# Kernel optimization log

Hardware: AMD Instinct MI355X
Metric: run time of the kernel (lower is better)

Reference implementation:

```python
import jax, jax.numpy as jnp
from jax import lax
import numpy as np

B, N, C, H, W = 32, 64, 16, 63, 63  # batch, num_bboxes, num_classes, output H/W


def _conv(x, w, b, s):
    y = lax.conv_general_dilated(x, w, (s, s), 'VALID',
                                 dimension_numbers=('NCHW', 'OIHW', 'NCHW'))
    return y + b[None, :, None, None]


def _bn(x, g, b, eps=1e-5):
    # BatchNorm2d in training mode: batch statistics, biased variance
    m = x.mean((0, 2, 3), keepdims=True)
    v = jnp.mean((x - m) ** 2, (0, 2, 3), keepdims=True)
    return g[None, :, None, None] * (x - m) * lax.rsqrt(v + eps) + b[None, :, None, None]


def _rectangle_render(x):
    # pixel grid flattened with w as the OUTER loop (ww repeated per h), matching torch code
    col = jnp.repeat(jnp.arange(W, dtype=jnp.int32), H)[None, :, None]  # [1,HW,1] x-coord
    row = jnp.tile(jnp.arange(H, dtype=jnp.int32), W)[None, :, None]    # [1,HW,1] y-coord
    c = x[:, :, :4].astype(jnp.int32)  # .long() truncation -> no grad through coords
    xL = c[:, None, :, 0]; yT = c[:, None, :, 1]
    xR = c[:, None, :, 2]; yB = c[:, None, :, 3]
    sub_xL = col - xL; sub_yT = row - yT
    sub_xR = col - xR; sub_yB = row - yB
    sub_y = yB - row;  sub_x = xR - col
    t1 = jnp.clip(sub_yT, 0, 1); t2 = jnp.clip(sub_y, 0, 1)  # relu then cap at 1
    F0 = jnp.maximum(1 - jnp.abs(sub_xL), 0) * t1 * t2
    F1 = jnp.maximum(1 - jnp.abs(sub_xR), 0) * t1 * t2
    t3 = jnp.clip(sub_xL, 0, 1); t4 = jnp.clip(sub_x, 0, 1)
    F2 = jnp.maximum(1 - jnp.abs(sub_yT), 0) * t3 * t4
    F3 = jnp.maximum(1 - jnp.abs(sub_yB), 0) * t3 * t4
    val = jnp.maximum(jnp.maximum(F0, F1), jnp.maximum(F2, F3)).astype(x.dtype)  # [B,HW,N]
    prod = x[:, None, :, 4:] * val[..., None]  # [B,HW,N,C]
    res = prod.max(axis=3)                      # [B,HW,N]
    # view(B,H,W,N).permute(0,1,3,2).permute(0,2,1,3) == reshape + transpose to [B,N,H,W]
    return res.reshape(x.shape[0], H, W, -1).transpose(0, 3, 1, 2)


def setup_inputs() -> dict:
    key = jax.random.key(0)
    ks = jax.random.split(key, 8)
    coords = jax.random.uniform(ks[0], (B, N, 4), jnp.float32) * (W - 1)
    probs = jax.random.uniform(ks[1], (B, N, C), jnp.float32)
    x = jnp.concatenate([coords, probs], axis=2)  # [B, N, 4+C]
    s = 0.05
    return {
        'x': x,
        'conv1_w': jax.random.normal(ks[2], (N, N, 3, 3), jnp.float32) * s,
        'conv1_b': jnp.zeros((N,), jnp.float32),
        'bn1_g': jnp.ones((N,), jnp.float32),
        'bn1_b': jnp.zeros((N,), jnp.float32),
        'conv2_w': jax.random.normal(ks[3], (2 * N, N, 3, 3), jnp.float32) * s,
        'conv2_b': jnp.zeros((2 * N,), jnp.float32),
        'bn2_g': jnp.ones((2 * N,), jnp.float32),
        'bn2_b': jnp.zeros((2 * N,), jnp.float32),
        'conv3_w': jax.random.normal(ks[4], (2 * N, 2 * N, 3, 3), jnp.float32) * s,
        'conv3_b': jnp.zeros((2 * N,), jnp.float32),
        'bn3_g': jnp.ones((2 * N,), jnp.float32),
        'bn3_b': jnp.zeros((2 * N,), jnp.float32),
        'fc1_w': jax.random.normal(ks[5], (N, 2 * N * 49), jnp.float32) * 0.02,
        'fc1_b': jnp.zeros((N,), jnp.float32),
        'fc2_w': jax.random.normal(ks[6], (1, N), jnp.float32) * 0.02,
        'fc2_b': jnp.zeros((1,), jnp.float32),
    }


def reference(x, conv1_w, conv1_b, bn1_g, bn1_b, conv2_w, conv2_b, bn2_g, bn2_b,
              conv3_w, conv3_b, bn3_g, bn3_b, fc1_w, fc1_b, fc2_w, fc2_b):
    layout = _rectangle_render(x)  # [B, N, H, W]
    out = jax.nn.relu(_bn(_conv(layout, conv1_w, conv1_b, 2), bn1_g, bn1_b))
    out = jax.nn.relu(_bn(_conv(out, conv2_w, conv2_b, 2), bn2_g, bn2_b))
    out = jax.nn.relu(_bn(_conv(out, conv3_w, conv3_b, 2), bn3_g, bn3_b))
    out = out.reshape(out.shape[0], -1)  # [B, 2N*49]
    out = jax.nn.relu(out @ fc1_w.T + fc1_b)
    out = out @ fc2_w.T + fc2_b
    return jax.nn.sigmoid(out)  # [B, 1]
```

## Files before the change

### kernel.cpp

```cpp
#include <hip/hip_runtime.h>
#include <math.h>

#define BB 32
#define NREC 64
#define CC 16
#define HW 63

typedef __attribute__((ext_vector_type(8))) short bf16x8;
typedef __attribute__((ext_vector_type(4))) short bf16x4;
typedef __attribute__((ext_vector_type(4))) float f32x4;

__device__ __forceinline__ unsigned short f2b(float x) {
    unsigned u = __float_as_uint(x);
    u += 0x7fffu + ((u >> 16) & 1u);
    return (unsigned short)(u >> 16);
}

__global__ __launch_bounds__(64) void render_nhwc_kernel(const float* __restrict__ x,
                                                         unsigned short* __restrict__ lay) {
    int b = blockIdx.x >> 6;
    int u = blockIdx.x & 63;
    int n = threadIdx.x;
    const float* xp = x + ((size_t)b * 64 + n) * 20;
    int xL = (int)xp[0], yT = (int)xp[1], xR = (int)xp[2], yB = (int)xp[3];
    float m = xp[4];
    #pragma unroll
    for (int c = 1; c < CC; ++c) m = fmaxf(m, xp[4 + c]);
    unsigned short mu = f2b(m);
    unsigned short* op = lay + (((size_t)b * 64 + u) * 64) * 64 + n;
    for (int v = 0; v < 64; ++v) {
        bool vb = (u < HW) && (v < HW) &&
                  (((u == xL || u == xR) && (v > yT && v < yB)) ||
                   ((v == yT || v == yB) && (u > xL && u < xR)));
        op[(size_t)v * 64] = vb ? mu : (unsigned short)0;
    }
}

__global__ __launch_bounds__(256) void wpack_kernel(const float* __restrict__ w,
                                                    unsigned short* __restrict__ wp,
                                                    int COUT, int CIN) {
    int K = CIN * 9;
    int idx = blockIdx.x * 256 + threadIdx.x;
    if (idx >= COUT * K) return;
    int co = idx / K, k = idx - co * K;
    int r = k / CIN, ci = k - r * CIN;
    wp[idx] = f2b(w[((size_t)co * CIN + ci) * 9 + r]);
}

template<int CIN, int COUT, int SR, int SC, int HOUT, int OCP, int RG, int RGP, int MGN>
__global__ __launch_bounds__(256) void gemmconv_kernel(
        const unsigned short* __restrict__ src,
        const unsigned short* __restrict__ wp,
        const float* __restrict__ bias,
        float* __restrict__ out) {
    constexpr int K   = 9 * CIN;
    constexpr int NTB = RGP * OCP / 16;
    constexpr int STR = 2 * RGP + 1;
    constexpr int STC = 2 * OCP + 1;
    constexpr int CIP = 36;
    constexpr int MTB = COUT / 16 / MGN;
    constexpr int NRG = (HOUT + RG - 1) / RG;

    __shared__ unsigned short stage[STR * STC * CIP];

    int tid = threadIdx.x;
    int wv = tid >> 6, lane = tid & 63;
    int l15 = lane & 15, lg = lane >> 4;
    int bid = blockIdx.x;
    int b  = bid & 31;
    int t2 = bid >> 5;
    int rg = t2 % NRG;
    int mg = t2 / NRG;
    int co0 = mg * (COUT / MGN);
    int mw = wv % MTB;

    f32x4 acc[NTB];
    #pragma unroll
    for (int i = 0; i < NTB; ++i) acc[i] = (f32x4){0.f, 0.f, 0.f, 0.f};

    const unsigned short* srcb = src + (size_t)b * SR * SC * CIN;
    int srow0 = 2 * rg * RG;

    for (int cb = 0; cb < CIN / 32; ++cb) {
        __syncthreads();
        for (int idx = tid; idx < STR * STC * 16; idx += 256) {
            int ci2 = idx & 15;
            int rc  = idx >> 4;
            int row = rc / STC, col = rc - row * STC;
            int srow = srow0 + row;
            unsigned v = 0;
            if (srow < SR && col < SC)
                v = *(const unsigned*)(srcb + ((size_t)srow * SC + col) * CIN + cb * 32 + ci2 * 2);
            *(unsigned*)(stage + (row * STC + col) * CIP + ci2 * 2) = v;
        }
        __syncthreads();
        #pragma unroll
        for (int r = 0; r < 9; ++r) {
            int ky = r / 3, kx = r % 3;
            int kk = r * CIN + cb * 32 + lg * 8;
            bf16x8 af = *(const bf16x8*)(wp + (size_t)(co0 + mw * 16 + l15) * K + kk);
            #pragma unroll
            for (int nt = 0; nt < NTB; ++nt) {
                int n = nt * 16 + l15;
                int dy = n / OCP, oxx = n % OCP;
                const unsigned short* sp =
                    stage + ((2 * dy + ky) * STC + (2 * oxx + kx)) * CIP + lg * 8;
                bf16x4 blo = *(const bf16x4*)sp;
                bf16x4 bhi = *(const bf16x4*)(sp + 4);
                bf16x8 bfr;
                bfr[0] = blo[0]; bfr[1] = blo[1]; bfr[2] = blo[2]; bfr[3] = blo[3];
                bfr[4] = bhi[0]; bfr[5] = bhi[1]; bfr[6] = bhi[2]; bfr[7] = bhi[3];
                acc[nt] = __builtin_amdgcn_mfma_f32_16x16x32_bf16(af, bfr, acc[nt], 0, 0, 0);
            }
        }
    }

    #pragma unroll
    for (int nt = 0; nt < NTB; ++nt) {
        int n = nt * 16 + l15;
        int oy = rg * RG + n / OCP, oxx = n % OCP;
        if (oy < HOUT && oxx < HOUT) {
            #pragma unroll
            for (int q = 0; q < 4; ++q) {
                int co = co0 + mw * 16 + lg * 4 + q;
                out[((size_t)b * COUT + co) * (HOUT * HOUT) + oy * HOUT + oxx] =
                    acc[nt][q] + bias[co];
            }
        }
    }
}

__global__ __launch_bounds__(256) void stats_part_kernel(
        const float* __restrict__ raw, float* __restrict__ psum,
        float* __restrict__ psq, int C, int HW2) {
    int c = blockIdx.x / BB;
    int b = blockIdx.x % BB;
    const float* rp = raw + ((size_t)b * C + c) * HW2;
    float s = 0.f, q = 0.f;
    for (int i = threadIdx.x; i < HW2; i += 256) {
        float v = rp[i];
        s += v; q += v * v;
    }
    __shared__ float rs[4], rq[4];
    int lane = threadIdx.x & 63, wv = threadIdx.x >> 6;
    #pragma unroll
    for (int o = 32; o > 0; o >>= 1) { s += __shfl_down(s, o, 64); q += __shfl_down(q, o, 64); }
    if (lane == 0) { rs[wv] = s; rq[wv] = q; }
    __syncthreads();
    if (threadIdx.x == 0) {
        psum[blockIdx.x] = rs[0] + rs[1] + rs[2] + rs[3];
        psq [blockIdx.x] = rq[0] + rq[1] + rq[2] + rq[3];
    }
}

__global__ void stats_fold_kernel(const float* __restrict__ psum,
                                  const float* __restrict__ psq,
                                  const float* __restrict__ g,
                                  const float* __restrict__ be,
                                  float* __restrict__ scale,
                                  float* __restrict__ shift,
                                  int C, float count) {
    int c = threadIdx.x + blockIdx.x * blockDim.x;
    if (c >= C) return;
    float S = 0.f, Q = 0.f;
    for (int b = 0; b < BB; ++b) { S += psum[c * BB + b]; Q += psq[c * BB + b]; }
    float mean = S / count;
    float var  = Q / count - mean * mean;
    float sc   = g[c] * rsqrtf(var + 1e-5f);
    scale[c] = sc;
    shift[c] = be[c] - mean * sc;
}

template<int C, int R, int SCo>
__global__ __launch_bounds__(256) void applyT_kernel(
        const float* __restrict__ raw, const float* __restrict__ scale,
        const float* __restrict__ shift, unsigned short* __restrict__ act) {
    int b = blockIdx.x / R, row = blockIdx.x % R;
    __shared__ float lds[C * (R + 2)];
    for (int idx = threadIdx.x; idx < C * R; idx += 256) {
        int ci = idx / R, col = idx - ci * R;
        float v = fmaxf(fmaf(raw[((size_t)b * C + ci) * (R * R) + row * R + col],
                             scale[ci], shift[ci]), 0.f);
        lds[ci * (R + 2) + col] = v;
    }
    __syncthreads();
    for (int idx = threadIdx.x; idx < SCo * C; idx += 256) {
        int col = idx / C, ci = idx - col * C;
        unsigned short v = 0;
        if (col < R) v = f2b(lds[ci * (R + 2) + col]);
        act[(((size_t)b * R + row) * SCo + col) * C + ci] = v;
    }
}

__global__ __launch_bounds__(64) void apply_kernel(
        const float* __restrict__ raw, const float* __restrict__ scale,
        const float* __restrict__ shift, float* __restrict__ act,
        int C, int HW2) {
    int bc = blockIdx.x;
    int c = bc % C;
    const float* rp = raw + (size_t)bc * HW2;
    float* ap = act + (size_t)bc * HW2;
    float s = scale[c], h = shift[c];
    for (int i = threadIdx.x; i < HW2; i += 64)
        ap[i] = fmaxf(fmaf(rp[i], s, h), 0.f);
}

__global__ __launch_bounds__(256) void fc1_kernel(
        const float* __restrict__ act3, const float* __restrict__ fc1w,
        const float* __restrict__ fc1b, float* __restrict__ h) {
    const int FLAT4 = 6272 / 4;
    int j = blockIdx.x >> 5;
    int b = blockIdx.x & 31;
    const float4* ip = (const float4*)(act3 + (size_t)b * 6272);
    const float4* wp = (const float4*)(fc1w + (size_t)j * 6272);
    float s = 0.f;
    for (int i = threadIdx.x; i < FLAT4; i += 256) {
        float4 xv = ip[i], wv = wp[i];
        s = fmaf(xv.x, wv.x, s); s = fmaf(xv.y, wv.y, s);
        s = fmaf(xv.z, wv.z, s); s = fmaf(xv.w, wv.w, s);
    }
    #pragma unroll
    for (int o = 32; o > 0; o >>= 1) s += __shfl_down(s, o, 64);
    __shared__ float red[4];
    if ((threadIdx.x & 63) == 0) red[threadIdx.x >> 6] = s;
    __syncthreads();
    if (threadIdx.x == 0) {
        float t = red[0] + red[1] + red[2] + red[3];
        h[b * 64 + j] = fmaxf(t + fc1b[j], 0.f);
    }
}

__global__ __launch_bounds__(64) void fc2_kernel(
        const float* __restrict__ h, const float* __restrict__ fc2w,
        const float* __restrict__ fc2b, float* __restrict__ outp) {
    int b = blockIdx.x;
    float v = h[b * 64 + threadIdx.x] * fc2w[threadIdx.x];
    #pragma unroll
    for (int o = 32; o > 0; o >>= 1) v += __shfl_down(v, o, 64);
    if (threadIdx.x == 0) outp[b] = 1.f / (1.f + expf(-(v + fc2b[0])));
}

extern "C" void kernel_launch(void* const* d_in, const int* in_sizes, int n_in,
                              void* d_out, int out_size, void* d_ws, size_t ws_size,
                              hipStream_t stream) {
    const float* x       = (const float*)d_in[0];
    const float* conv1_w = (const float*)d_in[1];
    const float* conv1_b = (const float*)d_in[2];
    const float* bn1_g   = (const float*)d_in[3];
    const float* bn1_b   = (const float*)d_in[4];
    const float* conv2_w = (const float*)d_in[5];
    const float* conv2_b = (const float*)d_in[6];
    const float* bn2_g   = (const float*)d_in[7];
    const float* bn2_b   = (const float*)d_in[8];
    const float* conv3_w = (const float*)d_in[9];
    const float* conv3_b = (const float*)d_in[10];
    const float* bn3_g   = (const float*)d_in[11];
    const float* bn3_b   = (const float*)d_in[12];
    const float* fc1_w   = (const float*)d_in[13];
    const float* fc1_b   = (const float*)d_in[14];
    const float* fc2_w   = (const float*)d_in[15];
    const float* fc2_b   = (const float*)d_in[16];
    float* out = (float*)d_out;

    char* wsc = (char*)d_ws;
    size_t o = 0;
    auto alloc = [&](size_t bytes) { char* p = wsc + o; o += (bytes + 255) & ~(size_t)255; return p; };
    unsigned short* laybf  = (unsigned short*)alloc((size_t)BB * 64 * 64 * 64 * 2);
    unsigned short* act1bf = (unsigned short*)alloc((size_t)BB * 31 * 32 * 64 * 2);
    unsigned short* act2bf = (unsigned short*)alloc((size_t)BB * 15 * 16 * 128 * 2);
    unsigned short* wp1    = (unsigned short*)alloc((size_t)64 * 576 * 2);
    unsigned short* wp2    = (unsigned short*)alloc((size_t)128 * 576 * 2);
    unsigned short* wp3    = (unsigned short*)alloc((size_t)128 * 1152 * 2);
    float* out1   = (float*)alloc((size_t)BB * 64 * 961 * 4);
    float* out2   = (float*)alloc((size_t)BB * 128 * 225 * 4);
    float* out3   = (float*)alloc((size_t)BB * 128 * 49 * 4);
    float* act3   = (float*)alloc((size_t)BB * 128 * 49 * 4);
    float* psum   = (float*)alloc((size_t)128 * BB * 4);
    float* psq    = (float*)alloc((size_t)128 * BB * 4);
    float* scale1 = (float*)alloc(64 * 4);
    float* shift1 = (float*)alloc(64 * 4);
    float* scale2 = (float*)alloc(128 * 4);
    float* shift2 = (float*)alloc(128 * 4);
    float* scale3 = (float*)alloc(128 * 4);
    float* shift3 = (float*)alloc(128 * 4);
    float* hbuf   = (float*)alloc((size_t)BB * 64 * 4);

    wpack_kernel<<<(64 * 576 + 255) / 256, 256, 0, stream>>>(conv1_w, wp1, 64, 64);
    wpack_kernel<<<(128 * 576 + 255) / 256, 256, 0, stream>>>(conv2_w, wp2, 128, 64);
    wpack_kernel<<<(128 * 1152 + 255) / 256, 256, 0, stream>>>(conv3_w, wp3, 128, 128);
    render_nhwc_kernel<<<BB * 64, 64, 0, stream>>>(x, laybf);

    gemmconv_kernel<64, 64, 64, 64, 31, 32, 2, 2, 1>
        <<<32 * 16, 256, 0, stream>>>(laybf, wp1, conv1_b, out1);
    stats_part_kernel<<<64 * BB, 256, 0, stream>>>(out1, psum, psq, 64, 961);
    stats_fold_kernel<<<1, 64, 0, stream>>>(psum, psq, bn1_g, bn1_b, scale1, shift1,
                                            64, (float)(BB * 961));
    applyT_kernel<64, 31, 32><<<BB * 31, 256, 0, stream>>>(out1, scale1, shift1, act1bf);

    gemmconv_kernel<64, 128, 31, 32, 15, 16, 2, 2, 2>
        <<<32 * 16, 256, 0, stream>>>(act1bf, wp2, conv2_b, out2);
    stats_part_kernel<<<128 * BB, 256, 0, stream>>>(out2, psum, psq, 128, 225);
    stats_fold_kernel<<<1, 128, 0, stream>>>(psum, psq, bn2_g, bn2_b, scale2, shift2,
                                             128, (float)(BB * 225));
    applyT_kernel<128, 15, 16><<<BB * 15, 256, 0, stream>>>(out2, scale2, shift2, act2bf);

    gemmconv_kernel<128, 128, 15, 16, 7, 8, 7, 8, 2>
        <<<32 * 2, 256, 0, stream>>>(act2bf, wp3, conv3_b, out3);
    stats_part_kernel<<<128 * BB, 256, 0, stream>>>(out3, psum, psq, 128, 49);
    stats_fold_kernel<<<1, 128, 0, stream>>>(psum, psq, bn3_g, bn3_b, scale3, shift3,
                                             128, (float)(BB * 49));
    apply_kernel<<<BB * 128, 64, 0, stream>>>(out3, scale3, shift3, act3, 128, 49);

    fc1_kernel<<<64 * 32, 256, 0, stream>>>(act3, fc1_w, fc1_b, hbuf);
    fc2_kernel<<<BB, 64, 0, stream>>>(hbuf, fc2_w, fc2_b, out);
}
```

Baseline: 117.1 us.

## Fuse BN stats into conv epilogue and BN apply into next conv's staging

Merges the render and weight-pack kernels into one prep launch. Each conv epilogue now computes per-channel partial sums and squares directly from the accumulators, which removes the separate stats pass. The BN scale/shift, ReLU and bf16 conversion are applied while staging the raw fp32 NCHW input of the next conv, and BN3 is folded into fc1, so the apply/transpose kernels and intermediate activation buffers go away. The cost is that staging now does strided fp32 NCHW loads with per-element scale/shift, and fc1 uses scalar loads with a division per element.

```diff
diff --git a/kernel.cpp b/kernel.cpp
--- a/kernel.cpp
+++ b/kernel.cpp
@@ -2,9 +2,6 @@
 #include <math.h>
 
 #define BB 32
-#define NREC 64
-#define CC 16
-#define HW 63
 
 typedef __attribute__((ext_vector_type(8))) short bf16x8;
 typedef __attribute__((ext_vector_type(4))) short bf16x4;
@@ -16,50 +13,71 @@
     return (unsigned short)(u >> 16);
 }
 
-__global__ __launch_bounds__(64) void render_nhwc_kernel(const float* __restrict__ x,
-                                                         unsigned short* __restrict__ lay) {
-    int b = blockIdx.x >> 6;
-    int u = blockIdx.x & 63;
-    int n = threadIdx.x;
-    const float* xp = x + ((size_t)b * 64 + n) * 20;
-    int xL = (int)xp[0], yT = (int)xp[1], xR = (int)xp[2], yB = (int)xp[3];
-    float m = xp[4];
-    #pragma unroll
-    for (int c = 1; c < CC; ++c) m = fmaxf(m, xp[4 + c]);
-    unsigned short mu = f2b(m);
-    unsigned short* op = lay + (((size_t)b * 64 + u) * 64) * 64 + n;
-    for (int v = 0; v < 64; ++v) {
-        bool vb = (u < HW) && (v < HW) &&
-                  (((u == xL || u == xR) && (v > yT && v < yB)) ||
-                   ((v == yT || v == yB) && (u > xL && u < xR)));
-        op[(size_t)v * 64] = vb ? mu : (unsigned short)0;
-    }
-}
-
-__global__ __launch_bounds__(256) void wpack_kernel(const float* __restrict__ w,
-                                                    unsigned short* __restrict__ wp,
-                                                    int COUT, int CIN) {
-    int K = CIN * 9;
-    int idx = blockIdx.x * 256 + threadIdx.x;
-    if (idx >= COUT * K) return;
-    int co = idx / K, k = idx - co * K;
-    int r = k / CIN, ci = k - r * CIN;
-    wp[idx] = f2b(w[((size_t)co * CIN + ci) * 9 + r]);
-}
-
-template<int CIN, int COUT, int SR, int SC, int HOUT, int OCP, int RG, int RGP, int MGN>
+__global__ __launch_bounds__(256) void prep_kernel(
+        const float* __restrict__ x, unsigned short* __restrict__ lay,
+        const float* __restrict__ w1, const float* __restrict__ w2,
+        const float* __restrict__ w3,
+        unsigned short* __restrict__ wp1, unsigned short* __restrict__ wp2,
+        unsigned short* __restrict__ wp3) {
+    int bid = blockIdx.x;
+    if (bid < 512) {
+        int b = bid >> 4;
+        int u = ((bid & 15) << 2) + (threadIdx.x >> 6);
+        int n = threadIdx.x & 63;
+        const float* xp = x + ((size_t)b * 64 + n) * 20;
+        int xL = (int)xp[0], yT = (int)xp[1], xR = (int)xp[2], yB = (int)xp[3];
+        float m = xp[4];
+        #pragma unroll
+        for (int c = 1; c < 16; ++c) m = fmaxf(m, xp[4 + c]);
+        unsigned short mu = f2b(m);
+        unsigned short* op = lay + (((size_t)b * 64 + u) * 64) * 64 + n;
+        #pragma unroll 4
+        for (int v = 0; v < 64; ++v) {
+            bool vb = (u < 63) && (v < 63) &&
+                      (((u == xL || u == xR) && (v > yT && v < yB)) ||
+                       ((v == yT || v == yB) && (u > xL && u < xR)));
+            op[(size_t)v * 64] = vb ? mu : (unsigned short)0;
+        }
+    } else {
+        int idx = (bid - 512) * 256 + threadIdx.x;
+        const int N1 = 64 * 576, N2 = 128 * 576, N3 = 128 * 1152;
+        if (idx < N1) {
+            int co = idx / 576, k = idx - co * 576;
+            int r = k / 64, ci = k - r * 64;
+            wp1[idx] = f2b(w1[((size_t)co * 64 + ci) * 9 + r]);
+        } else if (idx < N1 + N2) {
+            int i2 = idx - N1;
+            int co = i2 / 576, k = i2 - co * 576;
+            int r = k / 64, ci = k - r * 64;
+            wp2[i2] = f2b(w2[((size_t)co * 64 + ci) * 9 + r]);
+        } else if (idx < N1 + N2 + N3) {
+            int i3 = idx - N1 - N2;
+            int co = i3 / 1152, k = i3 - co * 1152;
+            int r = k / 128, ci = k - r * 128;
+            wp3[i3] = f2b(w3[((size_t)co * 128 + ci) * 9 + r]);
+        }
+    }
+}
+
+template<int CIN, int COUT, int SR, int SC, int HOUT, int OCP, int RG,
+         int RGP, int MGN, bool RAW>
 __global__ __launch_bounds__(256) void gemmconv_kernel(
-        const unsigned short* __restrict__ src,
+        const void* __restrict__ src_,
+        const float* __restrict__ scl,
+        const float* __restrict__ shf,
         const unsigned short* __restrict__ wp,
         const float* __restrict__ bias,
-        float* __restrict__ out) {
-    constexpr int K   = 9 * CIN;
-    constexpr int NTB = RGP * OCP / 16;
-    constexpr int STR = 2 * RGP + 1;
-    constexpr int STC = 2 * OCP + 1;
-    constexpr int CIP = 36;
-    constexpr int MTB = COUT / 16 / MGN;
-    constexpr int NRG = (HOUT + RG - 1) / RG;
+        float* __restrict__ out,
+        float* __restrict__ psum,
+        float* __restrict__ psq) {
+    constexpr int K    = 9 * CIN;
+    constexpr int NTB  = RGP * OCP / 16;
+    constexpr int STR  = 2 * RGP + 1;
+    constexpr int STC  = 2 * OCP + 1;
+    constexpr int CIP  = 36;
+    constexpr int MTB  = COUT / 16 / MGN;
+    constexpr int NRG  = (HOUT + RG - 1) / RG;
+    constexpr int PBLK = BB * NRG;
 
     __shared__ unsigned short stage[STR * STC * CIP];
 
@@ -78,20 +96,38 @@
     #pragma unroll
     for (int i = 0; i < NTB; ++i) acc[i] = (f32x4){0.f, 0.f, 0.f, 0.f};
 
-    const unsigned short* srcb = src + (size_t)b * SR * SC * CIN;
     int srow0 = 2 * rg * RG;
 
     for (int cb = 0; cb < CIN / 32; ++cb) {
         __syncthreads();
-        for (int idx = tid; idx < STR * STC * 16; idx += 256) {
-            int ci2 = idx & 15;
-            int rc  = idx >> 4;
-            int row = rc / STC, col = rc - row * STC;
-            int srow = srow0 + row;
-            unsigned v = 0;
-            if (srow < SR && col < SC)
-                v = *(const unsigned*)(srcb + ((size_t)srow * SC + col) * CIN + cb * 32 + ci2 * 2);
-            *(unsigned*)(stage + (row * STC + col) * CIP + ci2 * 2) = v;
+        if constexpr (RAW) {
+            const float* srcb = (const float*)src_ + (size_t)b * CIN * (SR * SC);
+            for (int idx = tid; idx < 32 * STR * STC; idx += 256) {
+                int ci = idx / (STR * STC);
+                int rc = idx - ci * (STR * STC);
+                int row = rc / STC, col = rc - row * STC;
+                int srow = srow0 + row;
+                int cig = cb * 32 + ci;
+                float v = 0.f;
+                if (srow < SR && col < SC)
+                    v = srcb[((size_t)cig * SR + srow) * SC + col];
+                v = fmaxf(fmaf(v, scl[cig], shf[cig]), 0.f);
+                stage[(row * STC + col) * CIP + ci] = f2b(v);
+            }
+        } else {
+            const unsigned short* srcb =
+                (const unsigned short*)src_ + (size_t)b * SR * SC * CIN;
+            for (int idx = tid; idx < STR * STC * 16; idx += 256) {
+                int ci2 = idx & 15;
+                int rc  = idx >> 4;
+                int row = rc / STC, col = rc - row * STC;
+                int srow = srow0 + row;
+                unsigned v = 0;
+                if (srow < SR && col < SC)
+                    v = *(const unsigned*)(srcb + ((size_t)srow * SC + col) * CIN
+                                           + cb * 32 + ci2 * 2);
+                *(unsigned*)(stage + (row * STC + col) * CIP + ci2 * 2) = v;
+            }
         }
         __syncthreads();
         #pragma unroll
@@ -115,41 +151,37 @@
         }
     }
 
+    float sa[4] = {0.f, 0.f, 0.f, 0.f}, qa[4] = {0.f, 0.f, 0.f, 0.f};
     #pragma unroll
     for (int nt = 0; nt < NTB; ++nt) {
         int n = nt * 16 + l15;
         int oy = rg * RG + n / OCP, oxx = n % OCP;
-        if (oy < HOUT && oxx < HOUT) {
-            #pragma unroll
-            for (int q = 0; q < 4; ++q) {
-                int co = co0 + mw * 16 + lg * 4 + q;
-                out[((size_t)b * COUT + co) * (HOUT * HOUT) + oy * HOUT + oxx] =
-                    acc[nt][q] + bias[co];
-            }
-        }
-    }
-}
-
-__global__ __launch_bounds__(256) void stats_part_kernel(
-        const float* __restrict__ raw, float* __restrict__ psum,
-        float* __restrict__ psq, int C, int HW2) {
-    int c = blockIdx.x / BB;
-    int b = blockIdx.x % BB;
-    const float* rp = raw + ((size_t)b * C + c) * HW2;
-    float s = 0.f, q = 0.f;
-    for (int i = threadIdx.x; i < HW2; i += 256) {
-        float v = rp[i];
-        s += v; q += v * v;
-    }
-    __shared__ float rs[4], rq[4];
-    int lane = threadIdx.x & 63, wv = threadIdx.x >> 6;
-    #pragma unroll
-    for (int o = 32; o > 0; o >>= 1) { s += __shfl_down(s, o, 64); q += __shfl_down(q, o, 64); }
-    if (lane == 0) { rs[wv] = s; rq[wv] = q; }
-    __syncthreads();
-    if (threadIdx.x == 0) {
-        psum[blockIdx.x] = rs[0] + rs[1] + rs[2] + rs[3];
-        psq [blockIdx.x] = rq[0] + rq[1] + rq[2] + rq[3];
+        bool act = (oy < HOUT) && (oxx < HOUT);
+        #pragma unroll
+        for (int q = 0; q < 4; ++q) {
+            int co = co0 + mw * 16 + lg * 4 + q;
+            float v = act ? (acc[nt][q] + bias[co]) : 0.f;
+            if (act)
+                out[((size_t)b * COUT + co) * (HOUT * HOUT) + oy * HOUT + oxx] = v;
+            sa[q] += v; qa[q] += v * v;
+        }
+    }
+    #pragma unroll
+    for (int o = 1; o < 16; o <<= 1) {
+        #pragma unroll
+        for (int q = 0; q < 4; ++q) {
+            sa[q] += __shfl_xor(sa[q], o, 64);
+            qa[q] += __shfl_xor(qa[q], o, 64);
+        }
+    }
+    if (l15 == 0) {
+        int pblk = b * NRG + rg;
+        #pragma unroll
+        for (int q = 0; q < 4; ++q) {
+            int co = co0 + mw * 16 + lg * 4 + q;
+            psum[(size_t)co * PBLK + pblk] = sa[q];
+            psq [(size_t)co * PBLK + pblk] = qa[q];
+        }
     }
 }
 
@@ -159,11 +191,14 @@
                                   const float* __restrict__ be,
                                   float* __restrict__ scale,
                                   float* __restrict__ shift,
-                                  int C, float count) {
+                                  int C, int PBLK, float count) {
     int c = threadIdx.x + blockIdx.x * blockDim.x;
     if (c >= C) return;
     float S = 0.f, Q = 0.f;
-    for (int b = 0; b < BB; ++b) { S += psum[c * BB + b]; Q += psq[c * BB + b]; }
+    for (int p = 0; p < PBLK; ++p) {
+        S += psum[(size_t)c * PBLK + p];
+        Q += psq[(size_t)c * PBLK + p];
+    }
     float mean = S / count;
     float var  = Q / count - mean * mean;
     float sc   = g[c] * rsqrtf(var + 1e-5f);
@@ -171,53 +206,21 @@
     shift[c] = be[c] - mean * sc;
 }
 
-template<int C, int R, int SCo>
-__global__ __launch_bounds__(256) void applyT_kernel(
-        const float* __restrict__ raw, const float* __restrict__ scale,
-        const float* __restrict__ shift, unsigned short* __restrict__ act) {
-    int b = blockIdx.x / R, row = blockIdx.x % R;
-    __shared__ float lds[C * (R + 2)];
-    for (int idx = threadIdx.x; idx < C * R; idx += 256) {
-        int ci = idx / R, col = idx - ci * R;
-        float v = fmaxf(fmaf(raw[((size_t)b * C + ci) * (R * R) + row * R + col],
-                             scale[ci], shift[ci]), 0.f);
-        lds[ci * (R + 2) + col] = v;
-    }
-    __syncthreads();
-    for (int idx = threadIdx.x; idx < SCo * C; idx += 256) {
-        int col = idx / C, ci = idx - col * C;
-        unsigned short v = 0;
-        if (col < R) v = f2b(lds[ci * (R + 2) + col]);
-        act[(((size_t)b * R + row) * SCo + col) * C + ci] = v;
-    }
-}
-
-__global__ __launch_bounds__(64) void apply_kernel(
-        const float* __restrict__ raw, const float* __restrict__ scale,
-        const float* __restrict__ shift, float* __restrict__ act,
-        int C, int HW2) {
-    int bc = blockIdx.x;
-    int c = bc % C;
-    const float* rp = raw + (size_t)bc * HW2;
-    float* ap = act + (size_t)bc * HW2;
-    float s = scale[c], h = shift[c];
-    for (int i = threadIdx.x; i < HW2; i += 64)
-        ap[i] = fmaxf(fmaf(rp[i], s, h), 0.f);
-}
-
 __global__ __launch_bounds__(256) void fc1_kernel(
-        const float* __restrict__ act3, const float* __restrict__ fc1w,
-        const float* __restrict__ fc1b, float* __restrict__ h) {
-    const int FLAT4 = 6272 / 4;
+        const float* __restrict__ out3,
+        const float* __restrict__ scale3, const float* __restrict__ shift3,
+        const float* __restrict__ fc1w,
+        const float* __restrict__ fc1b,
+        float* __restrict__ h) {
     int j = blockIdx.x >> 5;
     int b = blockIdx.x & 31;
-    const float4* ip = (const float4*)(act3 + (size_t)b * 6272);
-    const float4* wp = (const float4*)(fc1w + (size_t)j * 6272);
+    const float* ip = out3 + (size_t)b * 6272;
+    const float* wp = fc1w + (size_t)j * 6272;
     float s = 0.f;
-    for (int i = threadIdx.x; i < FLAT4; i += 256) {
-        float4 xv = ip[i], wv = wp[i];
-        s = fmaf(xv.x, wv.x, s); s = fmaf(xv.y, wv.y, s);
-        s = fmaf(xv.z, wv.z, s); s = fmaf(xv.w, wv.w, s);
+    for (int i = threadIdx.x; i < 6272; i += 256) {
+        int c = i / 49;
+        float xv = fmaxf(fmaf(ip[i], scale3[c], shift3[c]), 0.f);
+        s = fmaf(xv, wp[i], s);
     }
     #pragma unroll
     for (int o = 32; o > 0; o >>= 1) s += __shfl_down(s, o, 64);
@@ -265,18 +268,15 @@
     char* wsc = (char*)d_ws;
     size_t o = 0;
     auto alloc = [&](size_t bytes) { char* p = wsc + o; o += (bytes + 255) & ~(size_t)255; return p; };
-    unsigned short* laybf  = (unsigned short*)alloc((size_t)BB * 64 * 64 * 64 * 2);
-    unsigned short* act1bf = (unsigned short*)alloc((size_t)BB * 31 * 32 * 64 * 2);
-    unsigned short* act2bf = (unsigned short*)alloc((size_t)BB * 15 * 16 * 128 * 2);
-    unsigned short* wp1    = (unsigned short*)alloc((size_t)64 * 576 * 2);
-    unsigned short* wp2    = (unsigned short*)alloc((size_t)128 * 576 * 2);
-    unsigned short* wp3    = (unsigned short*)alloc((size_t)128 * 1152 * 2);
+    unsigned short* laybf = (unsigned short*)alloc((size_t)BB * 64 * 64 * 64 * 2);
+    unsigned short* wp1   = (unsigned short*)alloc((size_t)64 * 576 * 2);
+    unsigned short* wp2   = (unsigned short*)alloc((size_t)128 * 576 * 2);
+    unsigned short* wp3   = (unsigned short*)alloc((size_t)128 * 1152 * 2);
     float* out1   = (float*)alloc((size_t)BB * 64 * 961 * 4);
     float* out2   = (float*)alloc((size_t)BB * 128 * 225 * 4);
     float* out3   = (float*)alloc((size_t)BB * 128 * 49 * 4);
-    float* act3   = (float*)alloc((size_t)BB * 128 * 49 * 4);
-    float* psum   = (float*)alloc((size_t)128 * BB * 4);
-    float* psq    = (float*)alloc((size_t)128 * BB * 4);
+    float* psum   = (float*)alloc((size_t)128 * 512 * 4);
+    float* psq    = (float*)alloc((size_t)128 * 512 * 4);
     float* scale1 = (float*)alloc(64 * 4);
     float* shift1 = (float*)alloc(64 * 4);
     float* scale2 = (float*)alloc(128 * 4);
@@ -285,32 +285,31 @@
     float* shift3 = (float*)alloc(128 * 4);
     float* hbuf   = (float*)alloc((size_t)BB * 64 * 4);
 
-    wpack_kernel<<<(64 * 576 + 255) / 256, 256, 0, stream>>>(conv1_w, wp1, 64, 64);
-    wpack_kernel<<<(128 * 576 + 255) / 256, 256, 0, stream>>>(conv2_w, wp2, 128, 64);
-    wpack_kernel<<<(128 * 1152 + 255) / 256, 256, 0, stream>>>(conv3_w, wp3, 128, 128);
-    render_nhwc_kernel<<<BB * 64, 64, 0, stream>>>(x, laybf);
-
-    gemmconv_kernel<64, 64, 64, 64, 31, 32, 2, 2, 1>
-        <<<32 * 16, 256, 0, stream>>>(laybf, wp1, conv1_b, out1);
-    stats_part_kernel<<<64 * BB, 256, 0, stream>>>(out1, psum, psq, 64, 961);
-    stats_fold_kernel<<<1, 64, 0, stream>>>(psum, psq, bn1_g, bn1_b, scale1, shift1,
-                                            64, (float)(BB * 961));
-    applyT_kernel<64, 31, 32><<<BB * 31, 256, 0, stream>>>(out1, scale1, shift1, act1bf);
-
-    gemmconv_kernel<64, 128, 31, 32, 15, 16, 2, 2, 2>
-        <<<32 * 16, 256, 0, stream>>>(act1bf, wp2, conv2_b, out2);
-    stats_part_kernel<<<128 * BB, 256, 0, stream>>>(out2, psum, psq, 128, 225);
-    stats_fold_kernel<<<1, 128, 0, stream>>>(psum, psq, bn2_g, bn2_b, scale2, shift2,
-                                             128, (float)(BB * 225));
-    applyT_kernel<128, 15, 16><<<BB * 15, 256, 0, stream>>>(out2, scale2, shift2, act2bf);
-
-    gemmconv_kernel<128, 128, 15, 16, 7, 8, 7, 8, 2>
-        <<<32 * 2, 256, 0, stream>>>(act2bf, wp3, conv3_b, out3);
-    stats_part_kernel<<<128 * BB, 256, 0, stream>>>(out3, psum, psq, 128, 49);
-    stats_fold_kernel<<<1, 128, 0, stream>>>(psum, psq, bn3_g, bn3_b, scale3, shift3,
-                                             128, (float)(BB * 49));
-    apply_kernel<<<BB * 128, 64, 0, stream>>>(out3, scale3, shift3, act3, 128, 49);
-
-    fc1_kernel<<<64 * 32, 256, 0, stream>>>(act3, fc1_w, fc1_b, hbuf);
+    prep_kernel<<<1520, 256, 0, stream>>>(x, laybf, conv1_w, conv2_w, conv3_w,
+                                          wp1, wp2, wp3);
+
+    gemmconv_kernel<64, 64, 64, 64, 31, 32, 2, 2, 1, false>
+        <<<32 * 16, 256, 0, stream>>>(laybf, nullptr, nullptr, wp1, conv1_b,
+                                      out1, psum, psq);
+    stats_fold_kernel<<<1, 64, 0, stream>>>(psum, psq, bn1_g, bn1_b,
+                                            scale1, shift1, 64, 32 * 16,
+                                            (float)(BB * 961));
+
+    gemmconv_kernel<64, 128, 31, 31, 15, 16, 2, 2, 2, true>
+        <<<32 * 16, 256, 0, stream>>>(out1, scale1, shift1, wp2, conv2_b,
+                                      out2, psum, psq);
+    stats_fold_kernel<<<1, 128, 0, stream>>>(psum, psq, bn2_g, bn2_b,
+                                             scale2, shift2, 128, 32 * 8,
+                                             (float)(BB * 225));
+
+    gemmconv_kernel<128, 128, 15, 15, 7, 8, 7, 8, 2, true>
+        <<<32 * 2, 256, 0, stream>>>(out2, scale2, shift2, wp3, conv3_b,
+                                     out3, psum, psq);
+    stats_fold_kernel<<<1, 128, 0, stream>>>(psum, psq, bn3_g, bn3_b,
+                                             scale3, shift3, 128, 32 * 1,
+                                             (float)(BB * 49));
+
+    fc1_kernel<<<64 * 32, 256, 0, stream>>>(out3, scale3, shift3,
+                                            fc1_w, fc1_b, hbuf);
     fc2_kernel<<<BB, 64, 0, stream>>>(hbuf, fc2_w, fc2_b, out);
 }
```

Result: slower. 229.2 us (+95.7%).
